# Kernel tuning notes

Hardware: AMD Instinct MI355X
Metric: run time of the kernel (lower is better)

## Reference

```python
import jax, jax.numpy as jnp
import numpy as np

SEQ, D_IN, D_OUT = 8192, 1024, 1024

def setup_inputs() -> dict:
    key = jax.random.key(0)
    kx, kq, kk, kv = jax.random.split(key, 4)
    x = jax.random.normal(kx, (SEQ, D_IN), dtype=jnp.float32)
    # original uses torch.rand (uniform [0,1)) for parameters
    W_query = jax.random.uniform(kq, (D_IN, D_OUT), dtype=jnp.float32)
    W_key = jax.random.uniform(kk, (D_IN, D_OUT), dtype=jnp.float32)
    W_value = jax.random.uniform(kv, (D_IN, D_OUT), dtype=jnp.float32)
    return {"x": x, "W_query": W_query, "W_key": W_key, "W_value": W_value}

def reference(x, W_query, W_key, W_value):
    # x: [S, d_in]; projections: [S, d_out]
    queries = x @ W_query
    keys = x @ W_key
    values = x @ W_value
    scale = 1.0 / jnp.sqrt(jnp.asarray(keys.shape[-1], dtype=x.dtype))
    attn_scores = jnp.einsum('sd,td->st', queries, keys) * scale  # [S, S]
    attn_weights = jax.nn.softmax(attn_scores, axis=-1)
    context_vec = attn_weights @ values  # [S, d_out]
    return context_vec
```

## Files before the change

### kernel.cpp

```cpp
#include <hip/hip_runtime.h>
#include <hip/hip_bf16.h>
#include <hip/hip_fp16.h>

#define SEQ 8192
#define DM  1024

typedef __attribute__((ext_vector_type(8))) short    bf16x8;
typedef __attribute__((ext_vector_type(8))) _Float16 f16x8;
typedef __attribute__((ext_vector_type(4))) float    f32x4;

union H8 { _Float16 h[8]; int4 v; };

__device__ __forceinline__ unsigned short f2bf(float f) {
    union { float f; unsigned u; } x; x.f = f;
    unsigned r = x.u + 0x7fffu + ((x.u >> 16) & 1u);
    return (unsigned short)(r >> 16);
}
__device__ __forceinline__ float bf2f(unsigned short h) {
    union { unsigned u; float f; } x; x.u = ((unsigned)h) << 16;
    return x.f;
}

__device__ __forceinline__ void gld16(const unsigned short* g, unsigned short* l) {
    __builtin_amdgcn_global_load_lds(
        (const __attribute__((address_space(1))) void*)g,
        (__attribute__((address_space(3))) void*)l, 16, 0, 0);
}

__global__ __launch_bounds__(256) void prep_kernel(const float* __restrict__ x,
    unsigned short* __restrict__ xhi, unsigned short* __restrict__ xlo,
    float* __restrict__ rsum,
    const float* W0, const float* W1, const float* W2,
    unsigned short* Wqh, unsigned short* Wql,
    unsigned short* Wkh, unsigned short* Wkl,
    unsigned short* H2, unsigned short* L2)
{
    __shared__ float tile[64][65];
    __shared__ float rbuf[4];
    int t = threadIdx.x;

    if (blockIdx.x < 8192) {
        int base = blockIdx.x * 1024 + t * 4;
        float4 v = *(const float4*)(x + base);
        float f[4] = {v.x, v.y, v.z, v.w};
        unsigned short h[4], l[4];
#pragma unroll
        for (int j = 0; j < 4; j++) { h[j] = f2bf(f[j]); l[j] = f2bf(f[j] - bf2f(h[j])); }
        ushort4 hv = {h[0], h[1], h[2], h[3]};
        ushort4 lv = {l[0], l[1], l[2], l[3]};
        *(ushort4*)(xhi + base) = hv;
        *(ushort4*)(xlo + base) = lv;
        float s4 = f[0] + f[1] + f[2] + f[3];
#pragma unroll
        for (int sh = 1; sh < 64; sh <<= 1) s4 += __shfl_xor(s4, sh);
        if ((t & 63) == 0) rbuf[t >> 6] = s4;
        __syncthreads();
        if (t == 0) rsum[blockIdx.x] = rbuf[0] + rbuf[1] + rbuf[2] + rbuf[3];
        return;
    }

    if (blockIdx.x < 8192 + 2048) {
        int id = blockIdx.x - 8192;
        const float* W = (id < 1024) ? W0 : W1;
        unsigned short* H = (id < 1024) ? Wqh : Wkh;
        unsigned short* L = (id < 1024) ? Wql : Wkl;
        int base = (id & 1023) * 1024 + t * 4;
        float4 v = *(const float4*)(W + base);
        float f[4] = {v.x, v.y, v.z, v.w};
        unsigned short h[4], l[4];
#pragma unroll
        for (int j = 0; j < 4; j++) { h[j] = f2bf(f[j]); l[j] = f2bf(f[j] - bf2f(h[j])); }
        ushort4 hv = {h[0], h[1], h[2], h[3]};
        ushort4 lv = {l[0], l[1], l[2], l[3]};
        *(ushort4*)(H + base) = hv;
        *(ushort4*)(L + base) = lv;
        return;
    }

    int id2 = blockIdx.x - 10240;
    int bn = (id2 & 15) * 64;
    int bk = (id2 >> 4) * 64;
    const float* W = W2;

#pragma unroll
    for (int p = 0; p < 4; p++) {
        int r = p * 16 + (t >> 4);
        int c = (t & 15) * 4;
        float4 v = *(const float4*)(W + (size_t)(bk + r) * DM + bn + c);
        tile[r][c] = v.x; tile[r][c+1] = v.y; tile[r][c+2] = v.z; tile[r][c+3] = v.w;
    }
    __syncthreads();
#pragma unroll
    for (int p = 0; p < 2; p++) {
        int task = p * 256 + t;
        int rn = task >> 3;
        int kc = (task & 7) * 8;
        union { unsigned short u[8]; int4 v; } hh, ll;
#pragma unroll
        for (int j = 0; j < 8; j++) {
            float f = tile[kc + j][rn];
            hh.u[j] = f2bf(f);
            ll.u[j] = f2bf(f - bf2f(hh.u[j]));
        }
        size_t o = (size_t)(bn + rn) * DM + bk + kc;
        *(int4*)(H2 + o) = hh.v;
        *(int4*)(L2 + o) = ll.v;
    }
}

template<int MODE, int KD>
__global__ __launch_bounds__(256, 2) void gemm128(
    const unsigned short* A,   const unsigned short* Alo,
    const unsigned short* B_,  const unsigned short* Blo_,
    unsigned short* Chi, unsigned short* Clo,
    _Float16* Cf16, float* Cf32, const float* __restrict__ Scp)
{
    constexpr bool SPLIT = (MODE == 0 || MODE == 5);
    constexpr int NT = (MODE == 5) ? 4 : KD / 32;
    __shared__ alignas(16) unsigned short sAhi[2][128 * 32];
    __shared__ alignas(16) unsigned short sBhi[2][128 * 32];
    __shared__ alignas(16) unsigned short sAlo[SPLIT ? 2 * 128 * 32 : 16];
    __shared__ alignas(16) unsigned short sBlo[SPLIT ? 2 * 128 * 32 : 16];
    __shared__ alignas(16) _Float16 sSc[(MODE == 3) ? 128 * 130 : 8];

    const unsigned short* B   = B_;
    const unsigned short* Blo = Blo_;

    const int m0 = blockIdx.x * 128;
    const int n0 = blockIdx.y * 128;
    const int kbase = (MODE == 5) ? (int)blockIdx.z * 128 : 0;
    const int t = threadIdx.x;
    const int wave = t >> 6, lane = t & 63;
    const int wr = wave >> 1, wc = wave & 1;
    const int i16 = lane & 15, quad = lane >> 4;

    const int rs = wave * 32 + (lane >> 2);
    const int scol = ((lane & 3) ^ ((lane >> 3) & 3)) << 3;
    const size_t aoff = (size_t)(m0 + rs) * KD + scol;
    const size_t boff = (size_t)(n0 + rs) * KD + scol;
    const int ldsb = wave * 1024;

    int offA[4], offB[4];
#pragma unroll
    for (int mt = 0; mt < 4; mt++) {
        int row = wr * 64 + mt * 16 + i16;
        offA[mt] = row * 32 + ((quad ^ ((row >> 1) & 3)) << 3);
    }
#pragma unroll
    for (int nt = 0; nt < 4; nt++) {
        int row = wc * 64 + nt * 16 + i16;
        offB[nt] = row * 32 + ((quad ^ ((row >> 1) & 3)) << 3);
    }

    if constexpr (MODE == 3) {
#pragma unroll
        for (int i = 0; i < 16; i++) {
            int idx = i * 1024 + t * 4;
            int row = idx >> 7, col = idx & 127;
            float4 v = *(const float4*)(Scp + (size_t)(m0 + row) * 128 + col);
            _Float16* d = sSc + row * 130 + col;
            d[0] = (_Float16)v.x; d[1] = (_Float16)v.y;
            d[2] = (_Float16)v.z; d[3] = (_Float16)v.w;
        }
    }

    auto STAGE = [&](int buf, int k) {
        gld16(A + aoff + k,           sAhi[buf] + ldsb);
        gld16(A + aoff + 16 * KD + k, sAhi[buf] + ldsb + 512);
        gld16(B + boff + k,           sBhi[buf] + ldsb);
        gld16(B + boff + 16 * KD + k, sBhi[buf] + ldsb + 512);
        if constexpr (SPLIT) {
            gld16(Alo + aoff + k,           sAlo + buf * 4096 + ldsb);
            gld16(Alo + aoff + 16 * KD + k, sAlo + buf * 4096 + ldsb + 512);
            gld16(Blo + boff + k,           sBlo + buf * 4096 + ldsb);
            gld16(Blo + boff + 16 * KD + k, sBlo + buf * 4096 + ldsb + 512);
        }
    };

    f32x4 acc[4][4] = {};

    STAGE(0, kbase);
    __syncthreads();

    for (int kt = 0; kt < NT; ++kt) {
        const int cur = kt & 1;
        const int k = kbase + kt * 32;

        bf16x8 ahi[4], alo[4], bhi[4], blo[4];
#pragma unroll
        for (int mt = 0; mt < 4; mt++) {
            ahi[mt] = *(const bf16x8*)(sAhi[cur] + offA[mt]);
            if constexpr (SPLIT) alo[mt] = *(const bf16x8*)(sAlo + cur * 4096 + offA[mt]);
        }
#pragma unroll
        for (int nt = 0; nt < 4; nt++) {
            bhi[nt] = *(const bf16x8*)(sBhi[cur] + offB[nt]);
            if constexpr (SPLIT) blo[nt] = *(const bf16x8*)(sBlo + cur * 4096 + offB[nt]);
        }
        if constexpr (MODE == 3) {
#pragma unroll
            for (int mt = 0; mt < 4; mt++) {
                _Float16 sc = sSc[(wr * 64 + mt * 16 + i16) * 130 + (k >> 6)];
                f16x8 av = __builtin_bit_cast(f16x8, ahi[mt]);
                av = av * sc;
                ahi[mt] = __builtin_bit_cast(bf16x8, av);
            }
        }

        if (kt + 1 < NT) STAGE(cur ^ 1, k + 32);

        __builtin_amdgcn_s_setprio(1);
#pragma unroll
        for (int nt = 0; nt < 4; nt++)
#pragma unroll
            for (int mt = 0; mt < 4; mt++) {
                if constexpr (MODE == 3) {
                    acc[mt][nt] = __builtin_amdgcn_mfma_f32_16x16x32_f16(
                        __builtin_bit_cast(f16x8, ahi[mt]), __builtin_bit_cast(f16x8, bhi[nt]),
                        acc[mt][nt], 0, 0, 0);
                } else {
                    acc[mt][nt] = __builtin_amdgcn_mfma_f32_16x16x32_bf16(ahi[mt], bhi[nt], acc[mt][nt], 0, 0, 0);
                    if constexpr (SPLIT) {
                        acc[mt][nt] = __builtin_amdgcn_mfma_f32_16x16x32_bf16(ahi[mt], blo[nt], acc[mt][nt], 0, 0, 0);
                        acc[mt][nt] = __builtin_amdgcn_mfma_f32_16x16x32_bf16(alo[mt], bhi[nt], acc[mt][nt], 0, 0, 0);
                    }
                }
            }
        __builtin_amdgcn_s_setprio(0);

        asm volatile("s_waitcnt vmcnt(0)" ::: "memory");
        __builtin_amdgcn_s_barrier();
        __builtin_amdgcn_sched_barrier(0);
    }

    if constexpr (MODE == 0) {
#pragma unroll
        for (int mt = 0; mt < 4; mt++)
#pragma unroll
            for (int nt = 0; nt < 4; nt++)
#pragma unroll
                for (int r = 0; r < 4; r++) {
                    int row = m0 + wr * 64 + mt * 16 + quad * 4 + r;
                    int col = n0 + wc * 64 + nt * 16 + i16;
                    float v = acc[mt][nt][r];
                    unsigned short h = f2bf(v);
                    Chi[(size_t)row * DM + col] = h;
                    Clo[(size_t)row * DM + col] = f2bf(v - bf2f(h));
                }
    } else if constexpr (MODE == 1) {
#pragma unroll
        for (int mt = 0; mt < 4; mt++)
#pragma unroll
            for (int nt = 0; nt < 4; nt++) {
                int row0 = m0 + wr * 64 + mt * 16 + quad * 4;
                int col  = n0 + wc * 64 + nt * 16 + i16;
                union { _Float16 h[4]; unsigned long long q; } p;
#pragma unroll
                for (int r = 0; r < 4; r++) p.h[r] = (_Float16)acc[mt][nt][r];
                *(unsigned long long*)(Cf16 + (size_t)col * SEQ + row0) = p.q;
            }
    } else if constexpr (MODE == 5) {
        float* Gp = Cf32 + ((size_t)blockIdx.z << 20);
#pragma unroll
        for (int mt = 0; mt < 4; mt++)
#pragma unroll
            for (int nt = 0; nt < 4; nt++) {
                int row0 = m0 + wr * 64 + mt * 16 + quad * 4;
                int col  = n0 + wc * 64 + nt * 16 + i16;
                union { float f[4]; float4 v; } p;
#pragma unroll
                for (int r = 0; r < 4; r++) p.f[r] = acc[mt][nt][r];
                *(float4*)(Gp + (size_t)col * DM + row0) = p.v;
            }
    } else {
#pragma unroll
        for (int mt = 0; mt < 4; mt++)
#pragma unroll
            for (int nt = 0; nt < 4; nt++)
#pragma unroll
                for (int r = 0; r < 4; r++) {
                    int row = m0 + wr * 64 + mt * 16 + quad * 4 + r;
                    int col = n0 + wc * 64 + nt * 16 + i16;
                    Cf32[(size_t)row * DM + col] = acc[mt][nt][r];
                }
    }
}

__global__ __launch_bounds__(256) void greduce(const float* __restrict__ Gp,
    unsigned short* __restrict__ Ghi, unsigned short* __restrict__ Glo)
{
    int e = blockIdx.x;
    int d0 = threadIdx.x * 4;
    float s[4] = {0.f, 0.f, 0.f, 0.f};
#pragma unroll
    for (int z = 0; z < 8; z++) {
        float4 v = *(const float4*)(Gp + ((size_t)z << 20) + (size_t)e * DM + d0);
        s[0] += v.x; s[1] += v.y; s[2] += v.z; s[3] += v.w;
    }
    unsigned short h[4], l[4];
#pragma unroll
    for (int j = 0; j < 4; j++) {
        float f = s[j] - 256.0f;
        h[j] = f2bf(f);
        l[j] = f2bf(f - bf2f(h[j]));
    }
    ushort4 hv = {h[0], h[1], h[2], h[3]};
    ushort4 lv = {l[0], l[1], l[2], l[3]};
    *(ushort4*)(Ghi + (size_t)e * DM + d0) = hv;
    *(ushort4*)(Glo + (size_t)e * DM + d0) = lv;
}

__global__ __launch_bounds__(512, 2) void scores256(
    const unsigned short* __restrict__ Yh, const unsigned short* __restrict__ Yl,
    const unsigned short* __restrict__ Xh, const unsigned short* __restrict__ Xl,
    const float* __restrict__ rsum,
    _Float16* __restrict__ Eo, float* __restrict__ Tt, float* __restrict__ Zt)
{
    constexpr int KD = 1024;
    constexpr int NT = KD / 32;
    __shared__ alignas(16) unsigned short lds[2 * 4 * 8192];
    __shared__ float srM[256], srN[256];

    const int flat = blockIdx.y * gridDim.x + blockIdx.x;
    const int wg = (flat & 7) * 128 + (flat >> 3);
    const int m0 = (wg >> 5) << 8;
    const int n0 = (wg & 31) << 8;

    const int t = threadIdx.x;
    const int wave = t >> 6, lane = t & 63;
    const int wr = wave >> 2, wc = wave & 3;
    const int i16 = lane & 15, quad = lane >> 4;

    if (t < 256) srM[t] = rsum[m0 + t];
    else         srN[t - 256] = rsum[n0 + t - 256];

    const int srow = wave * 16 + (lane >> 2);
    const int scol = ((lane & 3) ^ ((lane >> 3) & 3)) << 3;
    const size_t ga = (size_t)(m0 + srow) * KD + scol;
    const size_t gb = (size_t)(n0 + srow) * KD + scol;
    const int ldw = wave * 512;

    int offA[8], offB[4];
#pragma unroll
    for (int mt = 0; mt < 8; mt++) {
        int row = wr * 128 + mt * 16 + i16;
        offA[mt] = row * 32 + ((quad ^ ((row >> 1) & 3)) << 3);
    }
#pragma unroll
    for (int nt = 0; nt < 4; nt++) {
        int row = wc * 64 + nt * 16 + i16;
        offB[nt] = row * 32 + ((quad ^ ((row >> 1) & 3)) << 3);
    }

    f32x4 acc[8][4] = {};

    auto STAGE = [&](int buf, int kt) {
        unsigned short* p = lds + buf * 32768;
        const int k = kt * 32;
#pragma unroll
        for (int i = 0; i < 2; i++) {
            const size_t gAo = ga + (size_t)(i * 128) * KD + k;
            const size_t gBo = gb + (size_t)(i * 128) * KD + k;
            const int lo = ldw + i * 4096;
            gld16(Yh + gAo, p + lo);
            gld16(Yl + gAo, p + 8192  + lo);
            gld16(Xh + gBo, p + 16384 + lo);
            gld16(Xl + gBo, p + 24576 + lo);
        }
    };

    STAGE(0, 0);
    asm volatile("s_waitcnt vmcnt(0)" ::: "memory");
    __builtin_amdgcn_s_barrier();
    __builtin_amdgcn_sched_barrier(0);

    for (int kt = 0; kt < NT; ++kt) {
        const int cur = kt & 1;
        const unsigned short* pAh = lds + cur * 32768;
        const unsigned short* pAl = pAh + 8192;
        const unsigned short* pBh = pAh + 16384;
        const unsigned short* pBl = pAh + 24576;

        bf16x8 ah[4], al[4], bh[4], bl[4];

#pragma unroll
        for (int mi = 0; mi < 4; mi++) {
            ah[mi] = *(const bf16x8*)(pAh + offA[mi]);
            al[mi] = *(const bf16x8*)(pAl + offA[mi]);
        }
#pragma unroll
        for (int ni = 0; ni < 4; ni++) {
            bh[ni] = *(const bf16x8*)(pBh + offB[ni]);
            bl[ni] = *(const bf16x8*)(pBl + offB[ni]);
        }
        if (kt + 1 < NT) STAGE(cur ^ 1, kt + 1);

        __builtin_amdgcn_s_setprio(1);
#pragma unroll
        for (int mi = 0; mi < 4; mi++)
#pragma unroll
            for (int ni = 0; ni < 4; ni++) {
                f32x4 c = acc[mi][ni];
                c = __builtin_amdgcn_mfma_f32_16x16x32_bf16(ah[mi], bh[ni], c, 0, 0, 0);
                c = __builtin_amdgcn_mfma_f32_16x16x32_bf16(ah[mi], bl[ni], c, 0, 0, 0);
                c = __builtin_amdgcn_mfma_f32_16x16x32_bf16(al[mi], bh[ni], c, 0, 0, 0);
                acc[mi][ni] = c;
            }
        __builtin_amdgcn_s_setprio(0);

#pragma unroll
        for (int mi = 0; mi < 4; mi++) {
            ah[mi] = *(const bf16x8*)(pAh + offA[4 + mi]);
            al[mi] = *(const bf16x8*)(pAl + offA[4 + mi]);
        }

        __builtin_amdgcn_s_setprio(1);
#pragma unroll
        for (int mi = 0; mi < 4; mi++)
#pragma unroll
            for (int ni = 0; ni < 4; ni++) {
                f32x4 c = acc[4 + mi][ni];
                c = __builtin_amdgcn_mfma_f32_16x16x32_bf16(ah[mi], bh[ni], c, 0, 0, 0);
                c = __builtin_amdgcn_mfma_f32_16x16x32_bf16(ah[mi], bl[ni], c, 0, 0, 0);
                c = __builtin_amdgcn_mfma_f32_16x16x32_bf16(al[mi], bh[ni], c, 0, 0, 0);
                acc[4 + mi][ni] = c;
            }
        __builtin_amdgcn_s_setprio(0);

        asm volatile("s_waitcnt vmcnt(0)" ::: "memory");
        __builtin_amdgcn_s_barrier();
        __builtin_amdgcn_sched_barrier(0);
    }

    const float scale = 0.03125f;
    const float RC = 8.0f;
    const int tix = (n0 + wc * 64) >> 6;
    const float rn0 = RC * srN[wc * 64 + i16];
    const float rn1 = RC * srN[wc * 64 + 16 + i16];
    const float rn2 = RC * srN[wc * 64 + 32 + i16];
    const float rn3 = RC * srN[wc * 64 + 48 + i16];
#pragma unroll
    for (int mt = 0; mt < 8; mt++)
#pragma unroll
        for (int r = 0; r < 4; r++) {
            float rm = srM[wr * 128 + mt * 16 + quad * 4 + r];
            float s0 = acc[mt][0][r] * scale + rm * rn0;
            float s1 = acc[mt][1][r] * scale + rm * rn1;
            float s2 = acc[mt][2][r] * scale + rm * rn2;
            float s3 = acc[mt][3][r] * scale + rm * rn3;
            float mx = fmaxf(fmaxf(s0, s1), fmaxf(s2, s3));
            mx = fmaxf(mx, __shfl_xor(mx, 1));
            mx = fmaxf(mx, __shfl_xor(mx, 2));
            mx = fmaxf(mx, __shfl_xor(mx, 4));
            mx = fmaxf(mx, __shfl_xor(mx, 8));
            float e0 = __expf(s0 - mx), e1 = __expf(s1 - mx);
            float e2 = __expf(s2 - mx), e3 = __expf(s3 - mx);
            float z = e0 + e1 + e2 + e3;
            z += __shfl_xor(z, 1);
            z += __shfl_xor(z, 2);
            z += __shfl_xor(z, 4);
            z += __shfl_xor(z, 8);
            int row = m0 + wr * 128 + mt * 16 + quad * 4 + r;
            if (i16 == 0) {
                Tt[(size_t)row * 128 + tix] = mx;
                Zt[(size_t)row * 128 + tix] = z;
            }
            size_t eb = (size_t)row * SEQ + n0 + wc * 64 + i16;
            Eo[eb +  0] = (_Float16)e0;
            Eo[eb + 16] = (_Float16)e1;
            Eo[eb + 32] = (_Float16)e2;
            Eo[eb + 48] = (_Float16)e3;
        }
}

__global__ __launch_bounds__(256) void sc_reduce(const float* __restrict__ Tt,
    const float* __restrict__ Zt, float* __restrict__ Sc)
{
    int row = blockIdx.x * 4 + (threadIdx.x >> 6);
    int lane = threadIdx.x & 63;
    size_t b = (size_t)row * 128 + lane;
    float t0 = Tt[b], t1 = Tt[b + 64];
    float z0 = Zt[b], z1 = Zt[b + 64];
    float m = fmaxf(t0, t1);
    for (int sh = 1; sh < 64; sh <<= 1) m = fmaxf(m, __shfl_xor(m, sh));
    float l = z0 * __expf(t0 - m) + z1 * __expf(t1 - m);
    for (int sh = 1; sh < 64; sh <<= 1) l += __shfl_xor(l, sh);
    float inv = 1.0f / l;
    Sc[b]      = __expf(t0 - m) * inv;
    Sc[b + 64] = __expf(t1 - m) * inv;
}

extern "C" void kernel_launch(void* const* d_in, const int* in_sizes, int n_in,
                              void* d_out, int out_size, void* d_ws, size_t ws_size,
                              hipStream_t stream)
{
    const float* x  = (const float*)d_in[0];
    const float* Wq = (const float*)d_in[1];
    const float* Wk = (const float*)d_in[2];
    const float* Wv = (const float*)d_in[3];
    float* Out = (float*)d_out;
    char* ws = (char*)d_ws;

    const size_t MB = 1024 * 1024;
    unsigned short* Wqh  = (unsigned short*)(ws + 0 * MB);
    unsigned short* Wql  = (unsigned short*)(ws + 2 * MB);
    unsigned short* Wkh  = (unsigned short*)(ws + 4 * MB);
    unsigned short* Wkl  = (unsigned short*)(ws + 6 * MB);
    unsigned short* Wvth = (unsigned short*)(ws + 8 * MB);
    unsigned short* Wvtl = (unsigned short*)(ws + 10 * MB);
    unsigned short* Ghi  = (unsigned short*)(ws + 12 * MB);
    unsigned short* Glo  = (unsigned short*)(ws + 14 * MB);
    float*          Gp   = (float*)        (ws + 16 * MB);
    _Float16*       E    = (_Float16*)     (ws + 0 * MB);

    size_t off = 128 * MB;
    unsigned short* Yhi = (unsigned short*)(ws + off); off += 16 * MB;
    unsigned short* Ylo = (unsigned short*)(ws + off); off += 16 * MB;
    unsigned short* xhi = (unsigned short*)(ws + off); off += 16 * MB;
    unsigned short* xlo = (unsigned short*)(ws + off); off += 16 * MB;
    _Float16*       Vt  = (_Float16*)      (ws + off); off += 16 * MB;
    float*          Tt  = (float*)         (ws + off); off += (size_t)SEQ * 128 * 4;
    float*          Zt  = (float*)         (ws + off); off += (size_t)SEQ * 128 * 4;
    float*          Sc  = (float*)         (ws + off); off += (size_t)SEQ * 128 * 4;
    float*          rs  = (float*)         (ws + off); off += (size_t)SEQ * 4;

    prep_kernel<<<8192 + 2048 + 256, 256, 0, stream>>>(x, xhi, xlo, rs, Wq, Wk, Wv,
        Wqh, Wql, Wkh, Wkl, Wvth, Wvtl);
    gemm128<5, DM><<<dim3(8, 8, 8), 256, 0, stream>>>(
        Wqh, Wql, Wkh, Wkl, nullptr, nullptr, nullptr, Gp, nullptr);
    greduce<<<1024, 256, 0, stream>>>(Gp, Ghi, Glo);
    gemm128<1, DM><<<dim3(SEQ / 128, DM / 128), 256, 0, stream>>>(
        xhi, nullptr, Wvth, nullptr, nullptr, nullptr, (_Float16*)Vt, nullptr, nullptr);
    gemm128<0, DM><<<dim3(SEQ / 128, DM / 128), 256, 0, stream>>>(
        xhi, xlo, Ghi, Glo, Yhi, Ylo, nullptr, nullptr, nullptr);
    scores256<<<dim3(SEQ / 256, SEQ / 256), 512, 0, stream>>>(
        Yhi, Ylo, xhi, xlo, rs, E, Tt, Zt);
    sc_reduce<<<SEQ / 4, 256, 0, stream>>>(Tt, Zt, Sc);
    gemm128<3, SEQ><<<dim3(SEQ / 128, DM / 128), 256, 0, stream>>>(
        (const unsigned short*)E, nullptr, (const unsigned short*)Vt, nullptr,
        nullptr, nullptr, nullptr, Out, Sc);
}
```

Baseline: 694.3 us.

## Use 1024-thread blocks in scores kernel with 64x64 per-wave tiles

Raises the scores256 block from 512 to 1024 threads (16 waves), so each wave computes a 64x64 sub-tile instead of 128x64 while the 256x256 block tile stays the same. Accumulator registers per wave are halved and each thread issues one global-to-LDS copy per operand per k-step instead of two. The cost is more waves contending at each barrier, more LDS fragment reads per MFMA, and the loss of the explicit two-blocks-per-CU occupancy hint.

```diff
diff --git a/kernel.cpp b/kernel.cpp
--- a/kernel.cpp
+++ b/kernel.cpp
@@ -310,7 +310,7 @@
     *(ushort4*)(Glo + (size_t)e * DM + d0) = lv;
 }
 
-__global__ __launch_bounds__(512, 2) void scores256(
+__global__ __launch_bounds__(1024) void scores256(
     const unsigned short* __restrict__ Yh, const unsigned short* __restrict__ Yl,
     const unsigned short* __restrict__ Xh, const unsigned short* __restrict__ Xl,
     const float* __restrict__ rsum,
@@ -332,7 +332,7 @@
     const int i16 = lane & 15, quad = lane >> 4;
 
     if (t < 256) srM[t] = rsum[m0 + t];
-    else         srN[t - 256] = rsum[n0 + t - 256];
+    else if (t < 512) srN[t - 256] = rsum[n0 + t - 256];
 
     const int srow = wave * 16 + (lane >> 2);
     const int scol = ((lane & 3) ^ ((lane >> 3) & 3)) << 3;
@@ -340,10 +340,10 @@
     const size_t gb = (size_t)(n0 + srow) * KD + scol;
     const int ldw = wave * 512;
 
-    int offA[8], offB[4];
-#pragma unroll
-    for (int mt = 0; mt < 8; mt++) {
-        int row = wr * 128 + mt * 16 + i16;
+    int offA[4], offB[4];
+#pragma unroll
+    for (int mt = 0; mt < 4; mt++) {
+        int row = wr * 64 + mt * 16 + i16;
         offA[mt] = row * 32 + ((quad ^ ((row >> 1) & 3)) << 3);
     }
 #pragma unroll
@@ -352,21 +352,15 @@
         offB[nt] = row * 32 + ((quad ^ ((row >> 1) & 3)) << 3);
     }
 
-    f32x4 acc[8][4] = {};
+    f32x4 acc[4][4] = {};
 
     auto STAGE = [&](int buf, int kt) {
         unsigned short* p = lds + buf * 32768;
         const int k = kt * 32;
-#pragma unroll
-        for (int i = 0; i < 2; i++) {
-            const size_t gAo = ga + (size_t)(i * 128) * KD + k;
-            const size_t gBo = gb + (size_t)(i * 128) * KD + k;
-            const int lo = ldw + i * 4096;
-            gld16(Yh + gAo, p + lo);
-            gld16(Yl + gAo, p + 8192  + lo);
-            gld16(Xh + gBo, p + 16384 + lo);
-            gld16(Xl + gBo, p + 24576 + lo);
-        }
+        gld16(Yh + ga + k, p + ldw);
+        gld16(Yl + ga + k, p + 8192  + ldw);
+        gld16(Xh + gb + k, p + 16384 + ldw);
+        gld16(Xl + gb + k, p + 24576 + ldw);
     };
 
     STAGE(0, 0);
@@ -381,13 +375,7 @@
         const unsigned short* pBh = pAh + 16384;
         const unsigned short* pBl = pAh + 24576;
 
-        bf16x8 ah[4], al[4], bh[4], bl[4];
-
-#pragma unroll
-        for (int mi = 0; mi < 4; mi++) {
-            ah[mi] = *(const bf16x8*)(pAh + offA[mi]);
-            al[mi] = *(const bf16x8*)(pAl + offA[mi]);
-        }
+        bf16x8 bh[4], bl[4];
 #pragma unroll
         for (int ni = 0; ni < 4; ni++) {
             bh[ni] = *(const bf16x8*)(pBh + offB[ni]);
@@ -397,34 +385,18 @@
 
         __builtin_amdgcn_s_setprio(1);
 #pragma unroll
-        for (int mi = 0; mi < 4; mi++)
+        for (int mi = 0; mi < 4; mi++) {
+            bf16x8 ah = *(const bf16x8*)(pAh + offA[mi]);
+            bf16x8 al = *(const bf16x8*)(pAl + offA[mi]);
 #pragma unroll
             for (int ni = 0; ni < 4; ni++) {
                 f32x4 c = acc[mi][ni];
-                c = __builtin_amdgcn_mfma_f32_16x16x32_bf16(ah[mi], bh[ni], c, 0, 0, 0);
-                c = __builtin_amdgcn_mfma_f32_16x16x32_bf16(ah[mi], bl[ni], c, 0, 0, 0);
-                c = __builtin_amdgcn_mfma_f32_16x16x32_bf16(al[mi], bh[ni], c, 0, 0, 0);
+                c = __builtin_amdgcn_mfma_f32_16x16x32_bf16(ah, bh[ni], c, 0, 0, 0);
+                c = __builtin_amdgcn_mfma_f32_16x16x32_bf16(ah, bl[ni], c, 0, 0, 0);
+                c = __builtin_amdgcn_mfma_f32_16x16x32_bf16(al, bh[ni], c, 0, 0, 0);
                 acc[mi][ni] = c;
             }
-        __builtin_amdgcn_s_setprio(0);
-
-#pragma unroll
-        for (int mi = 0; mi < 4; mi++) {
-            ah[mi] = *(const bf16x8*)(pAh + offA[4 + mi]);
-            al[mi] = *(const bf16x8*)(pAl + offA[4 + mi]);
-        }
-
-        __builtin_amdgcn_s_setprio(1);
-#pragma unroll
-        for (int mi = 0; mi < 4; mi++)
-#pragma unroll
-            for (int ni = 0; ni < 4; ni++) {
-                f32x4 c = acc[4 + mi][ni];
-                c = __builtin_amdgcn_mfma_f32_16x16x32_bf16(ah[mi], bh[ni], c, 0, 0, 0);
-                c = __builtin_amdgcn_mfma_f32_16x16x32_bf16(ah[mi], bl[ni], c, 0, 0, 0);
-                c = __builtin_amdgcn_mfma_f32_16x16x32_bf16(al[mi], bh[ni], c, 0, 0, 0);
-                acc[4 + mi][ni] = c;
-            }
+        }
         __builtin_amdgcn_s_setprio(0);
 
         asm volatile("s_waitcnt vmcnt(0)" ::: "memory");
@@ -440,10 +412,10 @@
     const float rn2 = RC * srN[wc * 64 + 32 + i16];
     const float rn3 = RC * srN[wc * 64 + 48 + i16];
 #pragma unroll
-    for (int mt = 0; mt < 8; mt++)
+    for (int mt = 0; mt < 4; mt++)
 #pragma unroll
         for (int r = 0; r < 4; r++) {
-            float rm = srM[wr * 128 + mt * 16 + quad * 4 + r];
+            float rm = srM[wr * 64 + mt * 16 + quad * 4 + r];
             float s0 = acc[mt][0][r] * scale + rm * rn0;
             float s1 = acc[mt][1][r] * scale + rm * rn1;
             float s2 = acc[mt][2][r] * scale + rm * rn2;
@@ -460,7 +432,7 @@
             z += __shfl_xor(z, 2);
             z += __shfl_xor(z, 4);
             z += __shfl_xor(z, 8);
-            int row = m0 + wr * 128 + mt * 16 + quad * 4 + r;
+            int row = m0 + wr * 64 + mt * 16 + quad * 4 + r;
             if (i16 == 0) {
                 Tt[(size_t)row * 128 + tix] = mx;
                 Zt[(size_t)row * 128 + tix] = z;
@@ -533,7 +505,7 @@
         xhi, nullptr, Wvth, nullptr, nullptr, nullptr, (_Float16*)Vt, nullptr, nullptr);
     gemm128<0, DM><<<dim3(SEQ / 128, DM / 128), 256, 0, stream>>>(
         xhi, xlo, Ghi, Glo, Yhi, Ylo, nullptr, nullptr, nullptr);
-    scores256<<<dim3(SEQ / 256, SEQ / 256), 512, 0, stream>>>(
+    scores256<<<dim3(SEQ / 256, SEQ / 256), 1024, 0, stream>>>(
         Yhi, Ylo, xhi, xlo, rs, E, Tt, Zt);
     sc_reduce<<<SEQ / 4, 256, 0, stream>>>(Tt, Zt, Sc);
     gemm128<3, SEQ><<<dim3(SEQ / 128, DM / 128), 256, 0, stream>>>(
```

Result: no change. 687.6 us (-1.0%).
